# Kernel tuning notes

Hardware: AMD Instinct MI355X
Metric: run time of the kernel (lower is better)

Reference implementation:

```python
import jax, jax.numpy as jnp
import numpy as np

NUM_HEADS = 16
THETA = 10000.0


def _apply_rope(x, pos):
    # x: [b, h, t, d_k], pos: [t] int
    d = x.shape[-1]
    inv_freq = THETA ** (-jnp.arange(0, d, 2, dtype=jnp.float32) / d)  # [d/2]
    ang = pos.astype(jnp.float32)[:, None] * inv_freq                  # [t, d/2]
    cos, sin = jnp.cos(ang), jnp.sin(ang)
    x1, x2 = x[..., ::2], x[..., 1::2]
    r1 = x1 * cos - x2 * sin
    r2 = x1 * sin + x2 * cos
    return jnp.stack([r1, r2], axis=-1).reshape(x.shape)


def setup_inputs() -> dict:
    key = jax.random.key(0)
    k1, k2, k3 = jax.random.split(key, 3)
    b, t, dm = 4, 2048, 2048
    in_features = jax.random.normal(k1, (b, t, dm), dtype=jnp.float32)
    token_positions = jnp.arange(t, dtype=jnp.int64)
    W_qkv = jax.random.normal(k2, (3 * dm, dm), dtype=jnp.float32) * 0.02
    W_o = jax.random.normal(k3, (dm, dm), dtype=jnp.float32) * 0.02
    return {"in_features": in_features, "token_positions": token_positions,
            "W_qkv": W_qkv, "W_o": W_o}


def reference(in_features, token_positions, W_qkv, W_o):
    b, t, dm = in_features.shape
    h = NUM_HEADS
    dk = dm // h
    # fused QKV projection (Linear: y = x W^T)
    qkv = in_features @ W_qkv.T                       # [b, t, 3*dm]
    q, k, v = jnp.split(qkv, 3, axis=-1)
    def to_heads(x):
        return x.reshape(b, t, h, dk).transpose(0, 2, 1, 3)  # [b, h, t, dk]
    q, k, v = to_heads(q), to_heads(k), to_heads(v)
    q = _apply_rope(q, token_positions)
    k = _apply_rope(k, token_positions)
    # causal SDPA
    scale = 1.0 / np.sqrt(dk).astype(np.float32)
    scores = jnp.einsum('bhqd,bhkd->bhqk', q, k) * scale
    causal = jnp.tril(jnp.ones((t, t), dtype=bool))
    scores = jnp.where(causal, scores, jnp.finfo(scores.dtype).min)
    attn = jax.nn.softmax(scores, axis=-1)
    out = jnp.einsum('bhqk,bhkd->bhqd', attn, v)      # [b, h, t, dk]
    out = out.transpose(0, 2, 1, 3).reshape(b, t, dm)
    return out @ W_o.T
```

## Files before the change

### kernel.cpp

```cpp
#include <hip/hip_runtime.h>

typedef unsigned short u16;
typedef __attribute__((ext_vector_type(8))) short s8v;
typedef __attribute__((ext_vector_type(8))) __bf16 bf8;
typedef __attribute__((ext_vector_type(4))) float f4v;

#define GLB(p) ((const __attribute__((address_space(1))) void*)(p))
#define LDS(p) ((__attribute__((address_space(3))) void*)(p))

static __device__ __forceinline__ float b2f(u16 u) {
    union { unsigned int i; float f; } v; v.i = ((unsigned int)u) << 16; return v.f;
}
static __device__ __forceinline__ u16 f2b(float f) {
    union { float f; unsigned int i; } v; v.f = f;
    v.i += 0x7fffu + ((v.i >> 16) & 1u);
    return (u16)(v.i >> 16);
}

__global__ __launch_bounds__(256) void k_conv(const float* __restrict__ in,
                                              u16* __restrict__ out, int n4) {
    int i = blockIdx.x * 256 + threadIdx.x;
    if (i >= n4) return;
    float4 v = ((const float4*)in)[i];
    union { u16 u[4]; unsigned long long ll; } o;
    o.u[0] = f2b(v.x); o.u[1] = f2b(v.y); o.u[2] = f2b(v.z); o.u[3] = f2b(v.w);
    ((unsigned long long*)out)[i] = o.ll;
}

template<int MODE>
__global__ __launch_bounds__(512, 2) void k_gemm_bt(
    const u16* __restrict__ A, const u16* __restrict__ B,
    int K, int N, int gx,
    u16* __restrict__ Qb, u16* __restrict__ Kb, u16* __restrict__ Vt,
    float* __restrict__ Cf)
{
    extern __shared__ __align__(16) u16 Ls[];

    const int t    = threadIdx.x;
    const int lane = t & 63;
    const int wid  = t >> 6;
    const int wm = wid >> 2, wn = wid & 3;
    const int la = lane & 15, lb = lane >> 4;

    const int bid = (int)blockIdx.x;
    const int id2 = (bid & 7) * ((int)gridDim.x >> 3) + (bid >> 3);
    const int bx = id2 % gx, by = id2 / gx;
    const long arow0 = (long)by * 256;
    const long brow0 = (long)bx * 256;

    const int srow = t >> 2;
    const int scol = ((((t & 3) * 16) ^ (((t >> 3) & 3) << 4)) >> 1);
    const u16* Asrc = A + (arow0 + srow) * (long)K + scol;
    const u16* Bsrc = B + (brow0 + srow) * (long)K + scol;
    const long rK128 = (long)128 * K;

#define STAGE(q_, js_) do {                                                     \
        const long ko_ = (long)(js_) * 32;                                      \
        u16* Lq_ = Ls + (q_) * 16384;                                           \
        __builtin_amdgcn_global_load_lds(GLB(Asrc + ko_),         LDS(Lq_ + t * 8),         16, 0, 0); \
        __builtin_amdgcn_global_load_lds(GLB(Asrc + rK128 + ko_), LDS(Lq_ + 4096 + t * 8),  16, 0, 0); \
        __builtin_amdgcn_global_load_lds(GLB(Bsrc + ko_),         LDS(Lq_ + 8192 + t * 8),  16, 0, 0); \
        __builtin_amdgcn_global_load_lds(GLB(Bsrc + rK128 + ko_), LDS(Lq_ + 12288 + t * 8), 16, 0, 0); \
    } while (0)

    f4v acc[8][4];
#pragma unroll
    for (int m = 0; m < 8; m++)
#pragma unroll
        for (int n = 0; n < 4; n++) acc[m][n] = (f4v){0.f, 0.f, 0.f, 0.f};

    const int NKT = K >> 5;
    STAGE(0, 0);
    STAGE(1, 1);
    STAGE(2, 2);
    asm volatile("s_waitcnt vmcnt(8)\n\ts_barrier" ::: "memory");

    const int fsw = (((lb * 16) ^ (((la >> 1) & 3) << 4)) >> 1);

    for (int jt = 0; jt < NKT; ++jt) {
        int js = jt + 3; if (js > NKT - 1) js = NKT - 1;
        STAGE(js & 3, js);

        const u16* Ac = Ls + (jt & 3) * 16384;
        const u16* Bc = Ac + 8192;
        bf8 af[8], bfr[4];
#pragma unroll
        for (int mi = 0; mi < 8; mi++)
            af[mi] = *(const bf8*)(Ac + (wm * 128 + mi * 16 + la) * 32 + fsw);
#pragma unroll
        for (int ni = 0; ni < 4; ni++)
            bfr[ni] = *(const bf8*)(Bc + (wn * 64 + ni * 16 + la) * 32 + fsw);

        __builtin_amdgcn_s_setprio(1);
#pragma unroll
        for (int mi = 0; mi < 8; mi++)
#pragma unroll
            for (int ni = 0; ni < 4; ni++)
                acc[mi][ni] = __builtin_amdgcn_mfma_f32_16x16x32_bf16(af[mi], bfr[ni], acc[mi][ni], 0, 0, 0);
        __builtin_amdgcn_s_setprio(0);

        asm volatile("s_waitcnt vmcnt(8)\n\ts_barrier" ::: "memory");
    }
#undef STAGE
    asm volatile("s_waitcnt vmcnt(0)" ::: "memory");

#pragma unroll
    for (int mi = 0; mi < 8; mi++) {
#pragma unroll
        for (int ni = 0; ni < 4; ni++) {
            const long grow0 = arow0 + wm * 128 + mi * 16 + lb * 4;
            const int  gcol  = (int)brow0 + wn * 64 + ni * 16 + la;
#pragma unroll
            for (int i = 0; i < 4; i++) {
                const float v = acc[mi][ni][i];
                const long r = grow0 + i;
                if (MODE == 0) {
                    const int part = gcol >> 11;
                    const int rem  = gcol & 2047;
                    const int head = rem >> 7, d = rem & 127;
                    const long bh = (r >> 11) * 16 + head;
                    const int tt = (int)(r & 2047);
                    if (part == 2) {
                        Vt[(bh << 18) + ((long)d << 11) + tt] = f2b(v);
                    } else {
                        u16* dst = (part == 0) ? Qb : Kb;
                        dst[((bh << 11) + tt) * 128 + d] = f2b(v);
                    }
                } else {
                    Cf[r * (long)N + gcol] = v;
                }
            }
        }
    }
}

__global__ __launch_bounds__(256) void k_rope(u16* __restrict__ Qb, u16* __restrict__ Kb,
                                              const int* __restrict__ pos) {
    const int idx = blockIdx.x * 256 + threadIdx.x;
    const int j  = idx & 63;
    const int t  = (idx >> 6) & 2047;
    const int bh = (idx >> 17) & 63;
    u16* P = (idx >> 23) ? Kb : Qb;
    const long off = ((((long)bh << 11) + t) << 7) + 2 * j;
    unsigned int raw = *(unsigned int*)(P + off);
    float x1 = b2f((u16)(raw & 0xffffu));
    float x2 = b2f((u16)(raw >> 16));
    float invf = exp2f((float)j * -0.20762050593046014f);
    float ang = (float)pos[t] * invf;
    float sn, cs;
    sincosf(ang, &sn, &cs);
    unsigned int o = (unsigned int)f2b(x1 * cs - x2 * sn)
                   | ((unsigned int)f2b(x1 * sn + x2 * cs) << 16);
    *(unsigned int*)(P + off) = o;
}

__global__ __launch_bounds__(512) void k_attn(const u16* __restrict__ Qb,
                                              const u16* __restrict__ Kb,
                                              const u16* __restrict__ Vt,
                                              u16* __restrict__ Ob)
{
    __shared__ __align__(16) u16 Ks[2][32 * 128];
    __shared__ __align__(16) u16 Vs[2][64 * 64];
    __shared__ __align__(16) u16 Pl[8][32 * 32];

    const int tid  = threadIdx.x;
    const int lane = tid & 63;
    const int w    = tid >> 6;
    const int la = lane & 15, lb = lane >> 4;
    const int qg = 7 - ((int)blockIdx.x >> 6);
    const int bh = blockIdx.x & 63;
    const long base = (long)bh << 18;
    const int qt = qg * 8 + w;
    const int q0 = qt * 32;
    const int tiles_w = qt + 1;
    const int NT = qg * 8 + 8;
    const float scale = 0.08838834764831845f;

    bf8 qf[2][4];
#pragma unroll
    for (int m = 0; m < 2; m++)
#pragma unroll
        for (int kb = 0; kb < 4; kb++)
            qf[m][kb] = *(const bf8*)(Qb + base + (long)(q0 + m * 16 + la) * 128 + kb * 32 + lb * 8);

    f4v o[2][8];
#pragma unroll
    for (int m = 0; m < 2; m++)
#pragma unroll
        for (int n = 0; n < 8; n++) o[m][n] = (f4v){0.f, 0.f, 0.f, 0.f};
    float lst[2][4];
#pragma unroll
    for (int m = 0; m < 2; m++)
#pragma unroll
        for (int i = 0; i < 4; i++) lst[m][i] = 0.f;

    char* Pb = (char*)(Pl[w]);

    const int ko = tid * 16;
    const int kr = ko >> 8, kc = (ko & 255) ^ ((kr & 7) << 4);
    const int vo = tid * 16;
    const int vR = vo >> 7, vc = (vo & 127) ^ ((vR & 7) << 4);
    const int vd = 2 * vR + (vc >> 6), vt = (vc & 63) >> 1;

#define STAGE(buf, jt_) do {                                                        \
        const int kv0_ = (jt_) * 32;                                               \
        __builtin_amdgcn_global_load_lds(                                          \
            GLB(Kb + base + (long)(kv0_ + kr) * 128 + (kc >> 1)),                  \
            LDS((u16*)Ks[buf] + tid * 8), 16, 0, 0);                               \
        __builtin_amdgcn_global_load_lds(                                          \
            GLB(Vt + base + ((long)vd << 11) + kv0_ + vt),                         \
            LDS((u16*)Vs[buf] + tid * 8), 16, 0, 0);                               \
    } while (0)

    STAGE(0, 0);

    for (int jt = 0; jt < NT; ++jt) {
        const int buf = jt & 1;
        __syncthreads();
        if (jt + 1 < NT) STAGE(buf ^ 1, jt + 1);

        if (jt < tiles_w) {
            const char* KsB = (const char*)Ks[buf];
            const char* VsB = (const char*)Vs[buf];

            f4v s[2][2];
            s[0][0] = s[0][1] = s[1][0] = s[1][1] = (f4v){0.f, 0.f, 0.f, 0.f};
#pragma unroll
            for (int n = 0; n < 2; n++) {
                const int row = n * 16 + la;
#pragma unroll
                for (int kb = 0; kb < 4; kb++) {
                    bf8 kf = *(const bf8*)(KsB + row * 256 + ((kb * 64 + lb * 16) ^ ((row & 7) << 4)));
                    s[0][n] = __builtin_amdgcn_mfma_f32_16x16x32_bf16(qf[0][kb], kf, s[0][n], 0, 0, 0);
                    s[1][n] = __builtin_amdgcn_mfma_f32_16x16x32_bf16(qf[1][kb], kf, s[1][n], 0, 0, 0);
                }
            }

            bf8 vf[8];
#pragma unroll
            for (int nO = 0; nO < 8; nO++) {
                const int R = nO * 8 + (la >> 1);
                vf[nO] = *(const bf8*)(VsB + R * 128 + (((la & 1) * 64 + lb * 16) ^ ((R & 7) << 4)));
            }

            const bool diag = (jt == qt);
            float p[2][2][4];
#pragma unroll
            for (int m = 0; m < 2; m++)
#pragma unroll
                for (int n = 0; n < 2; n++)
#pragma unroll
                    for (int i = 0; i < 4; i++) {
                        float v = __expf(fmaf(s[m][n][i], scale, -8.0f));
                        if (diag && (n * 16 + la) > (m * 16 + lb * 4 + i)) v = 0.f;
                        p[m][n][i] = v;
                        lst[m][i] += v;
                    }

#pragma unroll
            for (int m = 0; m < 2; m++)
#pragma unroll
                for (int n = 0; n < 2; n++)
#pragma unroll
                    for (int i = 0; i < 4; i++) {
                        const int row = m * 16 + lb * 4 + i;
                        const int colb = (n * 16 + la) * 2;
                        *(u16*)(Pb + row * 64 + (colb ^ ((row & 3) << 4))) = f2b(p[m][n][i]);
                    }
            bf8 pa[2];
#pragma unroll
            for (int am = 0; am < 2; am++) {
                const int row = am * 16 + la;
                pa[am] = *(const bf8*)(Pb + row * 64 + ((lb * 16) ^ ((row & 3) << 4)));
            }
#pragma unroll
            for (int nO = 0; nO < 8; nO++) {
                o[0][nO] = __builtin_amdgcn_mfma_f32_16x16x32_bf16(pa[0], vf[nO], o[0][nO], 0, 0, 0);
                o[1][nO] = __builtin_amdgcn_mfma_f32_16x16x32_bf16(pa[1], vf[nO], o[1][nO], 0, 0, 0);
            }
        }
        __syncthreads();
    }
#undef STAGE

    float linv[2][4];
#pragma unroll
    for (int m = 0; m < 2; m++)
#pragma unroll
        for (int i = 0; i < 4; i++) {
            float l = lst[m][i];
            l += __shfl_xor(l, 1);
            l += __shfl_xor(l, 2);
            l += __shfl_xor(l, 4);
            l += __shfl_xor(l, 8);
            linv[m][i] = 1.0f / l;
        }

    const int b = bh >> 4, h = bh & 15;
#pragma unroll
    for (int m = 0; m < 2; m++)
#pragma unroll
        for (int nO = 0; nO < 8; nO++)
#pragma unroll
            for (int i = 0; i < 4; i++) {
                const int row = q0 + m * 16 + lb * 4 + i;
                const int d = nO * 16 + la;
                Ob[((long)(b * 2048 + row) << 11) + h * 128 + d] = f2b(o[m][nO][i] * linv[m][i]);
            }
}

extern "C" void kernel_launch(void* const* d_in, const int* in_sizes, int n_in,
                              void* d_out, int out_size, void* d_ws, size_t ws_size,
                              hipStream_t stream)
{
    const float* X    = (const float*)d_in[0];
    const int*   pos  = (const int*)d_in[1];
    const float* Wqkv = (const float*)d_in[2];
    const float* Wo   = (const float*)d_in[3];
    float* out = (float*)d_out;

    char* ws = (char*)d_ws;
    u16* Xb    = (u16*)(ws + 0);
    u16* Wqkvb = (u16*)(ws + 33554432);
    u16* Wob   = (u16*)(ws + 58720256);
    u16* Qb    = (u16*)(ws + 67108864);
    u16* Kb    = (u16*)(ws + 100663296);
    u16* Vt    = (u16*)(ws + 134217728);
    u16* Ob    = (u16*)(ws + 167772160);

    k_conv<<<16384, 256, 0, stream>>>(X, Xb, 4194304);
    k_conv<<<12288, 256, 0, stream>>>(Wqkv, Wqkvb, 3145728);
    k_conv<<<4096, 256, 0, stream>>>(Wo, Wob, 1048576);
    k_gemm_bt<0><<<768, 512, 131072, stream>>>(Xb, Wqkvb, 2048, 6144, 24, Qb, Kb, Vt, nullptr);
    k_rope<<<65536, 256, 0, stream>>>(Qb, Kb, pos);
    k_attn<<<512, 512, 0, stream>>>(Qb, Kb, Vt, Ob);
    k_gemm_bt<1><<<256, 512, 131072, stream>>>(Ob, Wob, 2048, 2048, 8, nullptr, nullptr, nullptr, out);
}
```

Measured before the change: 487.0 us.

## Restructure GEMM mainloop into 64-wide K tiles with quadrant-interleaved LDS reads

The GEMM mainloop moves from a 4-stage ring of 32-wide K slices to a 2-stage double buffer of 64-wide K slices, with a new XOR swizzle on 16-byte groups. Each iteration is split into four MFMA quadrants, and LDS fragment reads for the next quadrant sit between barriers so reads overlap with matrix math. The goal is fewer barriers per K and better hiding of LDS latency behind MFMA work. In exchange, prefetch depth drops from three stages to one, which can expose global-load latency, and the many extra s_barriers add synchronisation cost.

```diff
diff --git a/kernel.cpp b/kernel.cpp
--- a/kernel.cpp
+++ b/kernel.cpp
@@ -48,20 +48,22 @@
     const long arow0 = (long)by * 256;
     const long brow0 = (long)bx * 256;
 
-    const int srow = t >> 2;
-    const int scol = ((((t & 3) * 16) ^ (((t >> 3) & 3) << 4)) >> 1);
-    const u16* Asrc = A + (arow0 + srow) * (long)K + scol;
-    const u16* Bsrc = B + (brow0 + srow) * (long)K + scol;
-    const long rK128 = (long)128 * K;
-
-#define STAGE(q_, js_) do {                                                     \
-        const long ko_ = (long)(js_) * 32;                                      \
-        u16* Lq_ = Ls + (q_) * 16384;                                           \
-        __builtin_amdgcn_global_load_lds(GLB(Asrc + ko_),         LDS(Lq_ + t * 8),         16, 0, 0); \
-        __builtin_amdgcn_global_load_lds(GLB(Asrc + rK128 + ko_), LDS(Lq_ + 4096 + t * 8),  16, 0, 0); \
-        __builtin_amdgcn_global_load_lds(GLB(Bsrc + ko_),         LDS(Lq_ + 8192 + t * 8),  16, 0, 0); \
-        __builtin_amdgcn_global_load_lds(GLB(Bsrc + rK128 + ko_), LDS(Lq_ + 12288 + t * 8), 16, 0, 0); \
+    const int sr = t >> 3;
+    const int sg = (t & 7) ^ (sr & 7);
+    const u16* Asrc = A + (arow0 + sr) * (long)K + sg * 8;
+    const u16* Bsrc = B + (brow0 + sr) * (long)K + sg * 8;
+    const long K64 = 64 * (long)K, K128 = 128 * (long)K;
+    u16* ldst = Ls + t * 8;
+
+#define STG(q_, op_, h_, kt_) do {                                              \
+        const u16* s_ = ((op_) ? Bsrc : Asrc) + (h_) * K128 + (long)(kt_) * 64; \
+        u16* d_ = ldst + (q_) * 32768 + (op_) * 16384 + (h_) * 4096 * 2;        \
+        __builtin_amdgcn_global_load_lds(GLB(s_),       LDS(d_),        16, 0, 0); \
+        __builtin_amdgcn_global_load_lds(GLB(s_ + K64), LDS(d_ + 4096), 16, 0, 0); \
     } while (0)
+#define BAR() asm volatile("s_barrier" ::: "memory")
+#define VM6() asm volatile("s_waitcnt vmcnt(6)" ::: "memory")
+#define RD(off) (*(const bf8*)(Ls + (off)))
 
     f4v acc[8][4];
 #pragma unroll
@@ -69,40 +71,97 @@
 #pragma unroll
         for (int n = 0; n < 4; n++) acc[m][n] = (f4v){0.f, 0.f, 0.f, 0.f};
 
-    const int NKT = K >> 5;
-    STAGE(0, 0);
-    STAGE(1, 1);
-    STAGE(2, 2);
-    asm volatile("s_waitcnt vmcnt(8)\n\ts_barrier" ::: "memory");
-
-    const int fsw = (((lb * 16) ^ (((la >> 1) & 3) << 4)) >> 1);
-
-    for (int jt = 0; jt < NKT; ++jt) {
-        int js = jt + 3; if (js > NKT - 1) js = NKT - 1;
-        STAGE(js & 3, js);
-
-        const u16* Ac = Ls + (jt & 3) * 16384;
-        const u16* Bc = Ac + 8192;
-        bf8 af[8], bfr[4];
-#pragma unroll
-        for (int mi = 0; mi < 8; mi++)
-            af[mi] = *(const bf8*)(Ac + (wm * 128 + mi * 16 + la) * 32 + fsw);
-#pragma unroll
-        for (int ni = 0; ni < 4; ni++)
-            bfr[ni] = *(const bf8*)(Bc + (wn * 64 + ni * 16 + la) * 32 + fsw);
-
+    const int r7 = la & 7;
+    const int gA0 = (lb ^ r7) * 8;
+    const int gA1 = ((lb ^ r7) ^ 4) * 8;
+    const int aRow = wm * 8192 + la * 64;
+    const int bRow = 16384 + (wn >> 1) * 8192 + ((wn & 1) * 64 + la) * 64;
+
+    const int NKT = K >> 6;
+    STG(0, 0, 0, 0); STG(0, 0, 1, 0); STG(0, 1, 0, 0); STG(0, 1, 1, 0);
+    asm volatile("s_waitcnt vmcnt(0)\n\ts_barrier" ::: "memory");
+
+    for (int X = 0; X < NKT; ++X) {
+        const int D = (X & 1) << 15;
+        const int q = (X + 1) & 1;
+        const int S = (X + 1 < NKT) ? X + 1 : NKT - 1;
+        bf8 aR[4][2], b0[2][2], b1[2][2];
+
+#pragma unroll
+        for (int mi = 0; mi < 4; mi++) {
+            aR[mi][0] = RD(D + aRow + mi * 1024 + gA0);
+            aR[mi][1] = RD(D + aRow + mi * 1024 + gA1);
+        }
+#pragma unroll
+        for (int nl = 0; nl < 2; nl++) {
+            b0[nl][0] = RD(D + bRow + nl * 1024 + gA0);
+            b0[nl][1] = RD(D + bRow + nl * 1024 + gA1);
+        }
+        STG(q, 0, 0, S); STG(q, 0, 1, S); STG(q, 1, 0, S); STG(q, 1, 1, S);
+        BAR();
         __builtin_amdgcn_s_setprio(1);
 #pragma unroll
-        for (int mi = 0; mi < 8; mi++)
-#pragma unroll
-            for (int ni = 0; ni < 4; ni++)
-                acc[mi][ni] = __builtin_amdgcn_mfma_f32_16x16x32_bf16(af[mi], bfr[ni], acc[mi][ni], 0, 0, 0);
+        for (int mi = 0; mi < 4; mi++)
+#pragma unroll
+            for (int nl = 0; nl < 2; nl++) {
+                acc[mi][nl] = __builtin_amdgcn_mfma_f32_16x16x32_bf16(aR[mi][0], b0[nl][0], acc[mi][nl], 0, 0, 0);
+                acc[mi][nl] = __builtin_amdgcn_mfma_f32_16x16x32_bf16(aR[mi][1], b0[nl][1], acc[mi][nl], 0, 0, 0);
+            }
         __builtin_amdgcn_s_setprio(0);
-
-        asm volatile("s_waitcnt vmcnt(8)\n\ts_barrier" ::: "memory");
+        BAR();
+
+#pragma unroll
+        for (int nl = 0; nl < 2; nl++) {
+            b1[nl][0] = RD(D + bRow + (2 + nl) * 1024 + gA0);
+            b1[nl][1] = RD(D + bRow + (2 + nl) * 1024 + gA1);
+        }
+        BAR();
+        __builtin_amdgcn_s_setprio(1);
+#pragma unroll
+        for (int mi = 0; mi < 4; mi++)
+#pragma unroll
+            for (int nl = 0; nl < 2; nl++) {
+                acc[mi][2 + nl] = __builtin_amdgcn_mfma_f32_16x16x32_bf16(aR[mi][0], b1[nl][0], acc[mi][2 + nl], 0, 0, 0);
+                acc[mi][2 + nl] = __builtin_amdgcn_mfma_f32_16x16x32_bf16(aR[mi][1], b1[nl][1], acc[mi][2 + nl], 0, 0, 0);
+            }
+        __builtin_amdgcn_s_setprio(0);
+        BAR();
+
+#pragma unroll
+        for (int mi = 0; mi < 4; mi++) {
+            aR[mi][0] = RD(D + aRow + (4 + mi) * 1024 + gA0);
+            aR[mi][1] = RD(D + aRow + (4 + mi) * 1024 + gA1);
+        }
+        BAR();
+        __builtin_amdgcn_s_setprio(1);
+#pragma unroll
+        for (int mi = 0; mi < 4; mi++)
+#pragma unroll
+            for (int nl = 0; nl < 2; nl++) {
+                acc[4 + mi][2 + nl] = __builtin_amdgcn_mfma_f32_16x16x32_bf16(aR[mi][0], b1[nl][0], acc[4 + mi][2 + nl], 0, 0, 0);
+                acc[4 + mi][2 + nl] = __builtin_amdgcn_mfma_f32_16x16x32_bf16(aR[mi][1], b1[nl][1], acc[4 + mi][2 + nl], 0, 0, 0);
+            }
+        __builtin_amdgcn_s_setprio(0);
+        BAR();
+
+        VM6();
+        BAR();
+        __builtin_amdgcn_s_setprio(1);
+#pragma unroll
+        for (int mi = 0; mi < 4; mi++)
+#pragma unroll
+            for (int nl = 0; nl < 2; nl++) {
+                acc[4 + mi][nl] = __builtin_amdgcn_mfma_f32_16x16x32_bf16(aR[mi][0], b0[nl][0], acc[4 + mi][nl], 0, 0, 0);
+                acc[4 + mi][nl] = __builtin_amdgcn_mfma_f32_16x16x32_bf16(aR[mi][1], b0[nl][1], acc[4 + mi][nl], 0, 0, 0);
+            }
+        __builtin_amdgcn_s_setprio(0);
+        BAR();
     }
-#undef STAGE
     asm volatile("s_waitcnt vmcnt(0)" ::: "memory");
+#undef STG
+#undef BAR
+#undef VM6
+#undef RD
 
 #pragma unroll
     for (int mi = 0; mi < 8; mi++) {
```

Result: no change. 486.7 us (-0.1%).
